# Kernel tuning notes

Measured on AMD Instinct MI355X. Metric: run time of the kernel, lower is better.

The kernel has to match this reference:

```python
import jax, jax.numpy as jnp
import numpy as np

C = 768  # in_channel == out_channel (required by conv9)

def _conv1x1(x, w, b):
    # x: [B,C,H,W], w: [O,C], b: [O]
    return jnp.einsum('bchw,oc->bohw', x, w) + b[None, :, None, None]

def _rot(x):
    # torch: gather with reversed index along dim 3, then permute(0,1,3,2)
    return jnp.swapaxes(jnp.flip(x, axis=3), 2, 3)

def _forward(hidden_states, Ws, bs):
    x = hidden_states
    B, Cc, W, H = x.shape
    o1 = _rot(x); o2 = _rot(o1); o3 = _rot(o2)
    hs11 = (jax.nn.relu(_conv1x1(x,  Ws[0], bs[0]))
          + jax.nn.relu(_conv1x1(o1, Ws[1], bs[1]))
          + jax.nn.relu(_conv1x1(o2, Ws[2], bs[2]))
          + jax.nn.relu(_conv1x1(o3, Ws[3], bs[3])))
    s = W // 2
    e1 = x[:, :, 0:s, 0:s]; e2 = x[:, :, 0:s, s:W]
    e3 = x[:, :, s:W, 0:s]; e4 = x[:, :, s:W, s:W]
    quads = [e1, e2, e3, e4]
    ts = []
    for _ in range(3):
        quads = [_rot(q) for q in quads]
        top = jnp.concatenate((quads[0], quads[1]), axis=-1)
        bot = jnp.concatenate((quads[2], quads[3]), axis=-1)
        ts.append(jnp.concatenate((top, bot), axis=-2))
    hs111 = (jax.nn.relu(_conv1x1(x,     Ws[4], bs[4]))
           + jax.nn.relu(_conv1x1(ts[0], Ws[5], bs[5]))
           + jax.nn.relu(_conv1x1(ts[1], Ws[6], bs[6]))
           + jax.nn.relu(_conv1x1(ts[2], Ws[7], bs[7])))
    # --- spatial matmul attention (per batch & channel, over HxW) ---
    q, k, v = hs11, hs111, hs11
    att = jnp.einsum('bcik,bckj->bcij', q, k)        # [B,C,W,W]
    attn = jax.nn.softmax(att, axis=-1)               # dropout = identity (eval)
    out = jnp.einsum('bcij,bcjh->bcih', attn, v)      # [B,C,W,H]
    out = jax.nn.relu(_conv1x1(out, Ws[8], bs[8]))    # proj dropout = identity (eval)
    return out

def setup_inputs() -> dict:
    key = jax.random.key(0)
    k1, k2, k3 = jax.random.split(key, 3)
    hidden_states = jax.random.normal(k1, (32, C, 32, 32), dtype=jnp.float32)
    # 9 Conv2d(C, C, kernel_size=1) layers -> stacked [9, O, C] weights and [9, O] biases
    fan_in = C
    bound = 1.0 / np.sqrt(fan_in)
    Ws = jax.random.uniform(k2, (9, C, C), minval=-bound, maxval=bound, dtype=jnp.float32)
    bs = jax.random.uniform(k3, (9, C), minval=-bound, maxval=bound, dtype=jnp.float32)
    return {"hidden_states": hidden_states, "Ws": Ws, "bs": bs}

def reference(hidden_states, Ws, bs):
    return _forward(hidden_states, Ws, bs)
```

## Files before the change

kernel.cpp:

```cpp
#include <hip/hip_runtime.h>
#include <hip/hip_fp16.h>

typedef unsigned short u16;
typedef float f32x4 __attribute__((ext_vector_type(4)));
typedef _Float16 half8 __attribute__((ext_vector_type(8)));
typedef unsigned short u16x4 __attribute__((ext_vector_type(4)));

#define CDIM 768
#define NP 1024
#define NB 32

static constexpr size_t CHW = (size_t)NB * CDIM * NP;

static constexpr size_t XT_OFF  = 0;
static constexpr size_t HS_OFF  = CHW * 2;
static constexpr size_t WHI_OFF = HS_OFF + CHW * 4;

__device__ __forceinline__ u16 f16bits(float f) {
  return __half_as_ushort(__float2half_rn(f));
}
__device__ __forceinline__ float f16tof(u16 b) {
  __half_raw hr; hr.x = b; return __half2float(__half(hr));
}

typedef __attribute__((address_space(1))) void gv_t;
typedef __attribute__((address_space(3))) void lv_t;
__device__ __forceinline__ void gload_lds16(const void* g, void* l) {
  __builtin_amdgcn_global_load_lds((gv_t*)g, (lv_t*)l, 16, 0, 0);
}

__global__ __launch_bounds__(256) void cast_w_k(const float* __restrict__ W,
                                                u16* __restrict__ hi) {
  int i = blockIdx.x * 256 + threadIdx.x;
  float4 v = ((const float4*)W)[i];
  u16x4 h4 = {f16bits(v.x), f16bits(v.y), f16bits(v.z), f16bits(v.w)};
  ((u16x4*)hi)[i] = h4;
}

__global__ __launch_bounds__(256) void transpose_f16_k(const float* __restrict__ src,
                                                       u16* __restrict__ dxt) {
  __shared__ float tle[32][33];
  const int b = blockIdx.z, c0 = blockIdx.y * 32, p0 = blockIdx.x * 32;
  const int tid = threadIdx.x;
  const int lr = tid >> 5, lc = tid & 31;
  const float* s = src + ((size_t)b * CDIM + c0) * NP + p0;
#pragma unroll
  for (int it = 0; it < 4; ++it) {
    int c = it * 8 + lr;
    tle[c][lc] = s[(size_t)c * NP + lc];
  }
  __syncthreads();
#pragma unroll
  for (int it = 0; it < 4; ++it) {
    int p = it * 8 + lr;
    float v = tle[lc][p];
    size_t off = ((size_t)b * NP + p0 + p) * CDIM + c0 + lc;
    dxt[off] = f16bits(v);
  }
}

__device__ __forceinline__ int sigma_fn(int mode, int z, int t, int p) {
  if (t == 0 || mode == 1) return p;
  int i = p >> 5, j = p & 31;
  if (z == 0) {
    if (t == 1) return (j << 5) | (31 - i);
    if (t == 2) return ((31 - i) << 5) | (31 - j);
    return ((31 - j) << 5) | i;
  } else {
    int ib = i & 16, jb = j & 16, il = i & 15, jl = j & 15;
    if (t == 1) return ((ib | jl) << 5) | (jb | (15 - il));
    if (t == 2) return ((ib | (15 - il)) << 5) | (jb | (15 - jl));
    return ((ib | (15 - jl)) << 5) | (jb | il);
  }
}

template <int OUTF16>
__global__ __launch_bounds__(512, 2) void gemm_p(
    const u16* __restrict__ Whi,
    const u16* __restrict__ Bx,
    const float* __restrict__ bias, void* __restrict__ dst,
    int nterms, int wselBase, int mode) {
  extern __shared__ u16 lds[];
  const int tid = threadIdx.x;
  const int lane = tid & 63;
  const int w = tid >> 6;
  const int wr = w >> 2, wc = w & 3;
  const int z = blockIdx.z;
  const int b = blockIdx.x >> 2;
  const int p0 = (blockIdx.x & 3) << 8;
  const int o0 = blockIdx.y << 7;
  const int l15 = lane & 15, l4 = lane >> 4;
  const int s7 = l15 & 7;
  float* blds = (float*)(lds + 73728);

  const int NSTEP = nterms * 12;

  const int baseA0 = (wr * 64 + l15) * 64 + ((l4) ^ s7) * 8;
  const int baseA1 = (wr * 64 + l15) * 64 + ((4 + l4) ^ s7) * 8;
  const int baseB0 = 8192 + (wc * 64 + l15) * 32 + (l4 ^ ((l15 >> 1) & 3)) * 8;
  const int baseB1 = baseB0 + 8192;

  int arow[2], acof[2];
#pragma unroll
  for (int it = 0; it < 2; ++it) {
    int d = it * 512 + tid;
    arow[it] = d >> 3;
    acof[it] = ((d & 7) ^ (arow[it] & 7)) * 8;
  }
  int brow[4], bcof[4];
#pragma unroll
  for (int it = 0; it < 4; ++it) {
    int d = it * 512 + tid;
    int h = d >> 10, rem = d & 1023;
    brow[it] = rem >> 2;
    bcof[it] = h * 32 + (((rem & 3) ^ ((brow[it] >> 1) & 3))) * 8;
  }

  const u16* aptr[2];
  const u16* bptr[4];
  auto setPtrs = [&](int term) {
    int wsel = wselBase + z * 4 + term;
#pragma unroll
    for (int it = 0; it < 2; ++it)
      aptr[it] = Whi + ((size_t)wsel * CDIM + o0 + arow[it]) * CDIM + acof[it];
#pragma unroll
    for (int it = 0; it < 4; ++it) {
      int srow = sigma_fn(mode, z, term, p0 + brow[it]);
      bptr[it] = Bx + ((size_t)b * NP + srow) * CDIM + bcof[it];
    }
  };

  if (tid < nterms * 128) {
    int t = tid >> 7, oo = tid & 127;
    blds[tid] = bias[(size_t)(wselBase + z * 4 + t) * CDIM + o0 + oo];
  }
  asm volatile("s_waitcnt lgkmcnt(0)" ::: "memory");

  f32x4 acc[4][4], racc[4][4];
#pragma unroll
  for (int m = 0; m < 4; ++m)
#pragma unroll
    for (int n = 0; n < 4; ++n) {
      acc[m][n] = (f32x4){0.f, 0.f, 0.f, 0.f};
      racc[m][n] = (f32x4){0.f, 0.f, 0.f, 0.f};
    }

  setPtrs(0);
#pragma unroll
  for (int it = 0; it < 2; ++it) gload_lds16(aptr[it], lds + (it * 512 + tid) * 8);
#pragma unroll
  for (int it = 0; it < 4; ++it) gload_lds16(bptr[it], lds + 8192 + (it * 512 + tid) * 8);
#pragma unroll
  for (int it = 0; it < 2; ++it) aptr[it] += 64;
#pragma unroll
  for (int it = 0; it < 4; ++it) bptr[it] += 64;
#pragma unroll
  for (int it = 0; it < 2; ++it) gload_lds16(aptr[it], lds + 24576 + (it * 512 + tid) * 8);
#pragma unroll
  for (int it = 0; it < 4; ++it) gload_lds16(bptr[it], lds + 24576 + 8192 + (it * 512 + tid) * 8);
#pragma unroll
  for (int it = 0; it < 2; ++it) aptr[it] += 64;
#pragma unroll
  for (int it = 0; it < 4; ++it) bptr[it] += 64;

  int nsk = 2, nst = 0;
  int ckk = 0, cterm = 0;
  int cur = 0, wb = 2;

  for (int s = 0; s < NSTEP; ++s) {
    if (s + 1 < NSTEP) {
      asm volatile("s_waitcnt vmcnt(6)" ::: "memory");
    } else {
      asm volatile("s_waitcnt vmcnt(0)" ::: "memory");
    }
    __builtin_amdgcn_s_barrier();
    asm volatile("" ::: "memory");

    const u16* la = lds + cur * 24576;
    u16* ldst = lds + wb * 24576;
    const bool dostage = (s + 2) < NSTEP;
    if (dostage && nsk == 12) { ++nst; nsk = 0; setPtrs(nst); }

    half8 ah[4], bb[4];
#pragma unroll
    for (int m = 0; m < 4; ++m) ah[m] = *(const half8*)(la + baseA0 + m * 1024);
#pragma unroll
    for (int n = 0; n < 4; ++n) bb[n] = *(const half8*)(la + baseB0 + n * 512);
    if (dostage) {
#pragma unroll
      for (int it = 0; it < 2; ++it) gload_lds16(aptr[it], ldst + (it * 512 + tid) * 8);
    }
    asm volatile("s_waitcnt lgkmcnt(0)" ::: "memory");
    __builtin_amdgcn_s_setprio(1);
#pragma unroll
    for (int m = 0; m < 4; ++m)
#pragma unroll
      for (int n = 0; n < 4; ++n)
        acc[m][n] = __builtin_amdgcn_mfma_f32_16x16x32_f16(ah[m], bb[n], acc[m][n], 0, 0, 0);
    __builtin_amdgcn_s_setprio(0);

#pragma unroll
    for (int m = 0; m < 4; ++m) ah[m] = *(const half8*)(la + baseA1 + m * 1024);
#pragma unroll
    for (int n = 0; n < 4; ++n) bb[n] = *(const half8*)(la + baseB1 + n * 512);
    if (dostage) {
#pragma unroll
      for (int it = 0; it < 4; ++it) gload_lds16(bptr[it], ldst + 8192 + (it * 512 + tid) * 8);
#pragma unroll
      for (int it = 0; it < 2; ++it) aptr[it] += 64;
#pragma unroll
      for (int it = 0; it < 4; ++it) bptr[it] += 64;
      ++nsk;
    }
    asm volatile("s_waitcnt lgkmcnt(0)" ::: "memory");
    __builtin_amdgcn_s_setprio(1);
#pragma unroll
    for (int m = 0; m < 4; ++m)
#pragma unroll
      for (int n = 0; n < 4; ++n)
        acc[m][n] = __builtin_amdgcn_mfma_f32_16x16x32_f16(ah[m], bb[n], acc[m][n], 0, 0, 0);
    __builtin_amdgcn_s_setprio(0);

    if (ckk == 11) {
#pragma unroll
      for (int m = 0; m < 4; ++m) {
        float4 bv = *(const float4*)&blds[cterm * 128 + wr * 64 + m * 16 + l4 * 4];
        float bvf[4] = {bv.x, bv.y, bv.z, bv.w};
#pragma unroll
        for (int n = 0; n < 4; ++n)
#pragma unroll
          for (int r = 0; r < 4; ++r) {
            racc[m][n][r] += fmaxf(0.f, acc[m][n][r] + bvf[r]);
            acc[m][n][r] = 0.f;
          }
      }
    }
    cur = cur == 2 ? 0 : cur + 1;
    wb = wb == 2 ? 0 : wb + 1;
    ++ckk; if (ckk == 12) { ckk = 0; ++cterm; }
  }

#pragma unroll
  for (int m = 0; m < 4; ++m) {
    int rowb = o0 + wr * 64 + m * 16 + l4 * 4;
#pragma unroll
    for (int n = 0; n < 4; ++n) {
      int col = p0 + wc * 64 + n * 16 + l15;
      size_t base = ((size_t)b * CDIM + rowb) * NP + col;
      if (OUTF16) {
        u16* dp = (u16*)dst + (size_t)z * CHW + base;
#pragma unroll
        for (int r = 0; r < 4; ++r) dp[(size_t)r * NP] = f16bits(racc[m][n][r]);
      } else {
        float* dp = (float*)dst + (size_t)z * CHW + base;
#pragma unroll
        for (int r = 0; r < 4; ++r) dp[(size_t)r * NP] = racc[m][n][r];
      }
    }
  }
}

__global__ __launch_bounds__(256) void attn_m_k(const u16* __restrict__ hs, u16* __restrict__ aoT) {
  __shared__ float q[4][1024];
  __shared__ float kk[4][1024];
  const int tid = threadIdx.x, w = tid >> 6, lane = tid & 63;
  const int pair0 = blockIdx.x * 4;
  const int b = pair0 / CDIM;
  const int c0 = pair0 % CDIM;
  const int l15 = lane & 15, l4 = lane >> 4;

#pragma unroll
  for (int it = 0; it < 8; ++it) {
    int d4 = it * 256 + tid;
    int pr = d4 >> 9;
    int mat = (d4 >> 8) & 1;
    int off4 = d4 & 255;
    ushort4 hv = *(const ushort4*)&hs[(size_t)mat * CHW + (size_t)(pair0 + pr) * NP + off4 * 4];
    float* dl = mat ? kk[pr] : q[pr];
    int off = off4 * 4;
    int row = off >> 5;
    int ph = ((off & 31) >> 2) ^ (row & 7) ^ (row >> 3);
    float4 v = {f16tof(hv.x), f16tof(hv.y), f16tof(hv.z), f16tof(hv.w)};
    *(float4*)&dl[row * 32 + ph * 4] = v;
  }
  __syncthreads();

  const float* Q = q[w];
  float* KK = kk[w];

  auto rd_row8 = [&](const float* M, int row) -> half8 {
    int rx = (row & 7) ^ (row >> 3);
    float4 a = *(const float4*)&M[row * 32 + ((2 * l4) ^ rx) * 4];
    float4 c = *(const float4*)&M[row * 32 + ((2 * l4 + 1) ^ rx) * 4];
    half8 h;
    h[0] = (_Float16)a.x; h[1] = (_Float16)a.y; h[2] = (_Float16)a.z; h[3] = (_Float16)a.w;
    h[4] = (_Float16)c.x; h[5] = (_Float16)c.y; h[6] = (_Float16)c.z; h[7] = (_Float16)c.w;
    return h;
  };
  auto rd_col8 = [&](const float* M, int col) -> half8 {
    half8 h;
#pragma unroll
    for (int e = 0; e < 8; ++e) {
      int row = l4 * 8 + e;
      int ph = (col >> 2) ^ (row & 7) ^ (row >> 3);
      h[e] = (_Float16)M[row * 32 + ph * 4 + (col & 3)];
    }
    return h;
  };

  half8 bq[2], akk[2];
#pragma unroll
  for (int it = 0; it < 2; ++it) bq[it] = rd_row8(Q, it * 16 + l15);
#pragma unroll
  for (int mh = 0; mh < 2; ++mh) akk[mh] = rd_col8(KK, mh * 16 + l15);
  f32x4 sacc[2][2];
#pragma unroll
  for (int mh = 0; mh < 2; ++mh)
#pragma unroll
    for (int it = 0; it < 2; ++it)
      sacc[mh][it] = __builtin_amdgcn_mfma_f32_16x16x32_f16(
          akk[mh], bq[it], (f32x4){0.f, 0.f, 0.f, 0.f}, 0, 0, 0);

#pragma unroll
  for (int it = 0; it < 2; ++it) {
    float mx = sacc[0][it][0];
#pragma unroll
    for (int r = 1; r < 4; ++r) mx = fmaxf(mx, sacc[0][it][r]);
#pragma unroll
    for (int r = 0; r < 4; ++r) mx = fmaxf(mx, sacc[1][it][r]);
    mx = fmaxf(mx, __shfl_xor(mx, 16));
    mx = fmaxf(mx, __shfl_xor(mx, 32));
    float pv[2][4];
    float sum = 0.f;
#pragma unroll
    for (int mh = 0; mh < 2; ++mh)
#pragma unroll
      for (int r = 0; r < 4; ++r) {
        pv[mh][r] = expf(sacc[mh][it][r] - mx);
        sum += pv[mh][r];
      }
    sum += __shfl_xor(sum, 16);
    sum += __shfl_xor(sum, 32);
    float inv = 1.f / sum;
    int row = it * 16 + l15;
    int rx = (row & 7) ^ (row >> 3);
#pragma unroll
    for (int mh = 0; mh < 2; ++mh) {
      float4 v = {pv[mh][0] * inv, pv[mh][1] * inv, pv[mh][2] * inv, pv[mh][3] * inv};
      *(float4*)&KK[row * 32 + ((mh * 4 + l4) ^ rx) * 4] = v;
    }
  }

  half8 bp[2], av[2];
#pragma unroll
  for (int it = 0; it < 2; ++it) bp[it] = rd_row8(KK, it * 16 + l15);
#pragma unroll
  for (int ht = 0; ht < 2; ++ht) av[ht] = rd_col8(Q, ht * 16 + l15);
  f32x4 oacc[2][2];
#pragma unroll
  for (int ht = 0; ht < 2; ++ht)
#pragma unroll
    for (int it = 0; it < 2; ++it)
      oacc[ht][it] = __builtin_amdgcn_mfma_f32_16x16x32_f16(
          av[ht], bp[it], (f32x4){0.f, 0.f, 0.f, 0.f}, 0, 0, 0);

#pragma unroll
  for (int it = 0; it < 2; ++it) {
    int row = it * 16 + l15;
    int rx = (row & 7) ^ (row >> 3);
#pragma unroll
    for (int ht = 0; ht < 2; ++ht) {
      float4 v = {oacc[ht][it][0], oacc[ht][it][1], oacc[ht][it][2], oacc[ht][it][3]};
      *(float4*)&KK[row * 32 + ((ht * 4 + l4) ^ rx) * 4] = v;
    }
  }
  __syncthreads();

#pragma unroll
  for (int it = 0; it < 4; ++it) {
    int p = it * 256 + tid;
    int row = p >> 5, col = p & 31;
    int idx = row * 32 + (((col >> 2) ^ (row & 7) ^ (row >> 3)) * 4) + (col & 3);
    ushort4 v;
    v.x = f16bits(kk[0][idx]);
    v.y = f16bits(kk[1][idx]);
    v.z = f16bits(kk[2][idx]);
    v.w = f16bits(kk[3][idx]);
    *(ushort4*)&aoT[((size_t)b * NP + p) * CDIM + c0] = v;
  }
}

extern "C" void kernel_launch(void* const* d_in, const int* in_sizes, int n_in,
                              void* d_out, int out_size, void* d_ws, size_t ws_size,
                              hipStream_t stream) {
  (void)in_sizes; (void)n_in; (void)out_size; (void)ws_size;
  const float* x = (const float*)d_in[0];
  const float* Ws = (const float*)d_in[1];
  const float* bs = (const float*)d_in[2];
  float* out = (float*)d_out;
  char* ws = (char*)d_ws;

  u16* XT  = (u16*)(ws + XT_OFF);
  u16* hs  = (u16*)(ws + HS_OFF);
  u16* Whi = (u16*)(ws + WHI_OFF);
  u16* aoT = (u16*)(ws + XT_OFF);

  cast_w_k<<<5184, 256, 0, stream>>>(Ws, Whi);
  transpose_f16_k<<<dim3(32, 24, 32), 256, 0, stream>>>(x, XT);
  gemm_p<1><<<dim3(128, 6, 2), 512, 149504, stream>>>(Whi, XT, bs, (void*)hs, 4, 0, 0);
  attn_m_k<<<6144, 256, 0, stream>>>(hs, aoT);
  gemm_p<0><<<dim3(128, 6, 1), 512, 149504, stream>>>(Whi, aoT, bs, (void*)out, 1, 8, 1);
}
```

Measured before the change: 508.5 us.

## Retile 1x1-conv GEMM to 256x256 blocks with K=32 stages and packed fp16 running sums

```diff
diff --git a/kernel.cpp b/kernel.cpp
--- a/kernel.cpp
+++ b/kernel.cpp
@@ -2,6 +2,7 @@
 #include <hip/hip_fp16.h>
 
 typedef unsigned short u16;
+typedef unsigned int u32;
 typedef float f32x4 __attribute__((ext_vector_type(4)));
 typedef _Float16 half8 __attribute__((ext_vector_type(8)));
 typedef unsigned short u16x4 __attribute__((ext_vector_type(4)));
@@ -21,6 +22,11 @@
 }
 __device__ __forceinline__ float f16tof(u16 b) {
   __half_raw hr; hr.x = b; return __half2float(__half(hr));
+}
+__device__ __forceinline__ u32 pk2(u32 p, float a, float b) {
+  float x = f16tof((u16)(p & 0xffff)) + a;
+  float y = f16tof((u16)(p >> 16)) + b;
+  return (u32)f16bits(x) | ((u32)f16bits(y) << 16);
 }
 
 typedef __attribute__((address_space(1))) void gv_t;
@@ -74,12 +80,12 @@
   }
 }
 
-template <int OUTF16>
-__global__ __launch_bounds__(512, 2) void gemm_p(
+template <int OUTF16, int NTERMS>
+__global__ __launch_bounds__(512, 2) void gemm_r(
     const u16* __restrict__ Whi,
     const u16* __restrict__ Bx,
     const float* __restrict__ bias, void* __restrict__ dst,
-    int nterms, int wselBase, int mode) {
+    int wselBase, int mode) {
   extern __shared__ u16 lds[];
   const int tid = threadIdx.x;
   const int lane = tid & 63;
@@ -88,80 +94,65 @@
   const int z = blockIdx.z;
   const int b = blockIdx.x >> 2;
   const int p0 = (blockIdx.x & 3) << 8;
-  const int o0 = blockIdx.y << 7;
+  const int o0 = blockIdx.y << 8;
   const int l15 = lane & 15, l4 = lane >> 4;
-  const int s7 = l15 & 7;
-  float* blds = (float*)(lds + 73728);
-
-  const int NSTEP = nterms * 12;
-
-  const int baseA0 = (wr * 64 + l15) * 64 + ((l4) ^ s7) * 8;
-  const int baseA1 = (wr * 64 + l15) * 64 + ((4 + l4) ^ s7) * 8;
-  const int baseB0 = 8192 + (wc * 64 + l15) * 32 + (l4 ^ ((l15 >> 1) & 3)) * 8;
-  const int baseB1 = baseB0 + 8192;
-
-  int arow[2], acof[2];
+  float* blds = (float*)(lds + 49152);
+  const int NSTEP = NTERMS * 24;
+
+  const int rA = wr * 128 + l15;
+  const int baseA = rA * 32 + (l4 ^ ((rA >> 1) & 3)) * 8;
+  const int rB = wc * 64 + l15;
+  const int baseB = 8192 + rB * 32 + (l4 ^ ((rB >> 1) & 3)) * 8;
+
+  int srow[2], scof[2];
 #pragma unroll
   for (int it = 0; it < 2; ++it) {
     int d = it * 512 + tid;
-    arow[it] = d >> 3;
-    acof[it] = ((d & 7) ^ (arow[it] & 7)) * 8;
-  }
-  int brow[4], bcof[4];
-#pragma unroll
-  for (int it = 0; it < 4; ++it) {
-    int d = it * 512 + tid;
-    int h = d >> 10, rem = d & 1023;
-    brow[it] = rem >> 2;
-    bcof[it] = h * 32 + (((rem & 3) ^ ((brow[it] >> 1) & 3))) * 8;
-  }
-
+    srow[it] = d >> 2;
+    scof[it] = ((d & 3) ^ ((srow[it] >> 1) & 3)) * 8;
+  }
   const u16* aptr[2];
-  const u16* bptr[4];
+  const u16* bptr[2];
   auto setPtrs = [&](int term) {
     int wsel = wselBase + z * 4 + term;
 #pragma unroll
-    for (int it = 0; it < 2; ++it)
-      aptr[it] = Whi + ((size_t)wsel * CDIM + o0 + arow[it]) * CDIM + acof[it];
-#pragma unroll
-    for (int it = 0; it < 4; ++it) {
-      int srow = sigma_fn(mode, z, term, p0 + brow[it]);
-      bptr[it] = Bx + ((size_t)b * NP + srow) * CDIM + bcof[it];
-    }
-  };
-
-  if (tid < nterms * 128) {
-    int t = tid >> 7, oo = tid & 127;
-    blds[tid] = bias[(size_t)(wselBase + z * 4 + t) * CDIM + o0 + oo];
-  }
+    for (int it = 0; it < 2; ++it) {
+      aptr[it] = Whi + ((size_t)wsel * CDIM + o0 + srow[it]) * CDIM + scof[it];
+      int srw = sigma_fn(mode, z, term, p0 + srow[it]);
+      bptr[it] = Bx + ((size_t)b * NP + srw) * CDIM + scof[it];
+    }
+  };
+  auto stageA = [&](u16* ldst) {
+    gload_lds16(aptr[0], ldst + tid * 8);
+    gload_lds16(aptr[1], ldst + 4096 + tid * 8);
+    aptr[0] += 32; aptr[1] += 32;
+  };
+  auto stageB = [&](u16* ldst) {
+    gload_lds16(bptr[0], ldst + 8192 + tid * 8);
+    gload_lds16(bptr[1], ldst + 12288 + tid * 8);
+    bptr[0] += 32; bptr[1] += 32;
+  };
+
+  for (int i = tid; i < NTERMS * 256; i += 512)
+    blds[i] = bias[(size_t)(wselBase + z * 4 + (i >> 8)) * CDIM + o0 + (i & 255)];
   asm volatile("s_waitcnt lgkmcnt(0)" ::: "memory");
 
-  f32x4 acc[4][4], racc[4][4];
-#pragma unroll
-  for (int m = 0; m < 4; ++m)
-#pragma unroll
-    for (int n = 0; n < 4; ++n) {
-      acc[m][n] = (f32x4){0.f, 0.f, 0.f, 0.f};
-      racc[m][n] = (f32x4){0.f, 0.f, 0.f, 0.f};
-    }
+  f32x4 acc[8][4];
+#pragma unroll
+  for (int mi = 0; mi < 8; ++mi)
+#pragma unroll
+    for (int ni = 0; ni < 4; ++ni) acc[mi][ni] = (f32x4){0.f, 0.f, 0.f, 0.f};
+  u32 rp[8][4][2];
+  if (NTERMS > 1) {
+#pragma unroll
+    for (int mi = 0; mi < 8; ++mi)
+#pragma unroll
+      for (int ni = 0; ni < 4; ++ni) { rp[mi][ni][0] = 0u; rp[mi][ni][1] = 0u; }
+  }
 
   setPtrs(0);
-#pragma unroll
-  for (int it = 0; it < 2; ++it) gload_lds16(aptr[it], lds + (it * 512 + tid) * 8);
-#pragma unroll
-  for (int it = 0; it < 4; ++it) gload_lds16(bptr[it], lds + 8192 + (it * 512 + tid) * 8);
-#pragma unroll
-  for (int it = 0; it < 2; ++it) aptr[it] += 64;
-#pragma unroll
-  for (int it = 0; it < 4; ++it) bptr[it] += 64;
-#pragma unroll
-  for (int it = 0; it < 2; ++it) gload_lds16(aptr[it], lds + 24576 + (it * 512 + tid) * 8);
-#pragma unroll
-  for (int it = 0; it < 4; ++it) gload_lds16(bptr[it], lds + 24576 + 8192 + (it * 512 + tid) * 8);
-#pragma unroll
-  for (int it = 0; it < 2; ++it) aptr[it] += 64;
-#pragma unroll
-  for (int it = 0; it < 4; ++it) bptr[it] += 64;
+  stageA(lds); stageB(lds);
+  stageA(lds + 16384); stageB(lds + 16384);
 
   int nsk = 2, nst = 0;
   int ckk = 0, cterm = 0;
@@ -169,92 +160,84 @@
 
   for (int s = 0; s < NSTEP; ++s) {
     if (s + 1 < NSTEP) {
-      asm volatile("s_waitcnt vmcnt(6)" ::: "memory");
+      asm volatile("s_waitcnt vmcnt(4)" ::: "memory");
     } else {
       asm volatile("s_waitcnt vmcnt(0)" ::: "memory");
     }
     __builtin_amdgcn_s_barrier();
     asm volatile("" ::: "memory");
 
-    const u16* la = lds + cur * 24576;
-    u16* ldst = lds + wb * 24576;
+    const u16* la = lds + cur * 16384;
+    u16* ldst = lds + wb * 16384;
     const bool dostage = (s + 2) < NSTEP;
-    if (dostage && nsk == 12) { ++nst; nsk = 0; setPtrs(nst); }
-
-    half8 ah[4], bb[4];
-#pragma unroll
-    for (int m = 0; m < 4; ++m) ah[m] = *(const half8*)(la + baseA0 + m * 1024);
-#pragma unroll
-    for (int n = 0; n < 4; ++n) bb[n] = *(const half8*)(la + baseB0 + n * 512);
-    if (dostage) {
-#pragma unroll
-      for (int it = 0; it < 2; ++it) gload_lds16(aptr[it], ldst + (it * 512 + tid) * 8);
-    }
+    if (dostage && nsk == 24) { ++nst; nsk = 0; setPtrs(nst); }
+
+    half8 af[4], bf[4];
+#pragma unroll
+    for (int n = 0; n < 4; ++n) bf[n] = *(const half8*)(la + baseB + n * 512);
+#pragma unroll
+    for (int m = 0; m < 4; ++m) af[m] = *(const half8*)(la + baseA + m * 512);
+    if (dostage) stageA(ldst);
     asm volatile("s_waitcnt lgkmcnt(0)" ::: "memory");
     __builtin_amdgcn_s_setprio(1);
 #pragma unroll
     for (int m = 0; m < 4; ++m)
 #pragma unroll
       for (int n = 0; n < 4; ++n)
-        acc[m][n] = __builtin_amdgcn_mfma_f32_16x16x32_f16(ah[m], bb[n], acc[m][n], 0, 0, 0);
+        acc[m][n] = __builtin_amdgcn_mfma_f32_16x16x32_f16(af[m], bf[n], acc[m][n], 0, 0, 0);
     __builtin_amdgcn_s_setprio(0);
 
 #pragma unroll
-    for (int m = 0; m < 4; ++m) ah[m] = *(const half8*)(la + baseA1 + m * 1024);
-#pragma unroll
-    for (int n = 0; n < 4; ++n) bb[n] = *(const half8*)(la + baseB1 + n * 512);
-    if (dostage) {
-#pragma unroll
-      for (int it = 0; it < 4; ++it) gload_lds16(bptr[it], ldst + 8192 + (it * 512 + tid) * 8);
-#pragma unroll
-      for (int it = 0; it < 2; ++it) aptr[it] += 64;
-#pragma unroll
-      for (int it = 0; it < 4; ++it) bptr[it] += 64;
-      ++nsk;
-    }
+    for (int m = 0; m < 4; ++m) af[m] = *(const half8*)(la + baseA + (4 + m) * 512);
+    if (dostage) { stageB(ldst); ++nsk; }
     asm volatile("s_waitcnt lgkmcnt(0)" ::: "memory");
     __builtin_amdgcn_s_setprio(1);
 #pragma unroll
     for (int m = 0; m < 4; ++m)
 #pragma unroll
       for (int n = 0; n < 4; ++n)
-        acc[m][n] = __builtin_amdgcn_mfma_f32_16x16x32_f16(ah[m], bb[n], acc[m][n], 0, 0, 0);
+        acc[4 + m][n] = __builtin_amdgcn_mfma_f32_16x16x32_f16(af[m], bf[n], acc[4 + m][n], 0, 0, 0);
     __builtin_amdgcn_s_setprio(0);
 
-    if (ckk == 11) {
-#pragma unroll
-      for (int m = 0; m < 4; ++m) {
-        float4 bv = *(const float4*)&blds[cterm * 128 + wr * 64 + m * 16 + l4 * 4];
-        float bvf[4] = {bv.x, bv.y, bv.z, bv.w};
-#pragma unroll
-        for (int n = 0; n < 4; ++n)
-#pragma unroll
-          for (int r = 0; r < 4; ++r) {
-            racc[m][n][r] += fmaxf(0.f, acc[m][n][r] + bvf[r]);
-            acc[m][n][r] = 0.f;
-          }
+    if (NTERMS > 1 && ckk == 23) {
+#pragma unroll
+      for (int mi = 0; mi < 8; ++mi) {
+        float4 bv = *(const float4*)&blds[cterm * 256 + wr * 128 + mi * 16 + l4 * 4];
+#pragma unroll
+        for (int ni = 0; ni < 4; ++ni) {
+          rp[mi][ni][0] = pk2(rp[mi][ni][0], fmaxf(0.f, acc[mi][ni][0] + bv.x),
+                                             fmaxf(0.f, acc[mi][ni][1] + bv.y));
+          rp[mi][ni][1] = pk2(rp[mi][ni][1], fmaxf(0.f, acc[mi][ni][2] + bv.z),
+                                             fmaxf(0.f, acc[mi][ni][3] + bv.w));
+          acc[mi][ni] = (f32x4){0.f, 0.f, 0.f, 0.f};
+        }
       }
     }
     cur = cur == 2 ? 0 : cur + 1;
     wb = wb == 2 ? 0 : wb + 1;
-    ++ckk; if (ckk == 12) { ckk = 0; ++cterm; }
-  }
-
-#pragma unroll
-  for (int m = 0; m < 4; ++m) {
-    int rowb = o0 + wr * 64 + m * 16 + l4 * 4;
-#pragma unroll
-    for (int n = 0; n < 4; ++n) {
-      int col = p0 + wc * 64 + n * 16 + l15;
+    ++ckk; if (ckk == 24) { ckk = 0; ++cterm; }
+  }
+
+#pragma unroll
+  for (int mi = 0; mi < 8; ++mi) {
+    int rowb = o0 + wr * 128 + mi * 16 + l4 * 4;
+#pragma unroll
+    for (int ni = 0; ni < 4; ++ni) {
+      int col = p0 + wc * 64 + ni * 16 + l15;
       size_t base = ((size_t)b * CDIM + rowb) * NP + col;
-      if (OUTF16) {
+      if (NTERMS > 1) {
         u16* dp = (u16*)dst + (size_t)z * CHW + base;
-#pragma unroll
-        for (int r = 0; r < 4; ++r) dp[(size_t)r * NP] = f16bits(racc[m][n][r]);
+        dp[0 * NP] = (u16)(rp[mi][ni][0] & 0xffff);
+        dp[1 * NP] = (u16)(rp[mi][ni][0] >> 16);
+        dp[2 * NP] = (u16)(rp[mi][ni][1] & 0xffff);
+        dp[3 * NP] = (u16)(rp[mi][ni][1] >> 16);
       } else {
+        float4 bv = *(const float4*)&blds[wr * 128 + mi * 16 + l4 * 4];
+        float bvf[4] = {bv.x, bv.y, bv.z, bv.w};
         float* dp = (float*)dst + (size_t)z * CHW + base;
 #pragma unroll
-        for (int r = 0; r < 4; ++r) dp[(size_t)r * NP] = racc[m][n][r];
+        for (int r = 0; r < 4; ++r)
+          dp[(size_t)r * NP] = fmaxf(0.f, acc[mi][ni][r] + bvf[r]);
       }
     }
   }
@@ -407,7 +390,7 @@
 
   cast_w_k<<<5184, 256, 0, stream>>>(Ws, Whi);
   transpose_f16_k<<<dim3(32, 24, 32), 256, 0, stream>>>(x, XT);
-  gemm_p<1><<<dim3(128, 6, 2), 512, 149504, stream>>>(Whi, XT, bs, (void*)hs, 4, 0, 0);
+  gemm_r<1, 4><<<dim3(128, 3, 2), 512, 102400, stream>>>(Whi, XT, bs, (void*)hs, 0, 0);
   attn_m_k<<<6144, 256, 0, stream>>>(hs, aoT);
-  gemm_p<0><<<dim3(128, 6, 1), 512, 149504, stream>>>(Whi, aoT, bs, (void*)out, 1, 8, 1);
-}
+  gemm_r<0, 1><<<dim3(128, 3, 1), 512, 99328, stream>>>(Whi, aoT, bs, (void*)out, 8, 1);
+}
```

Measured after the change: 503.9 us. No clear change (-0.9%).

## Block activations into 16-channel panels, rewrite attention and add dedicated final GEMM

Applied to the files above, without the earlier changes.

```diff
diff --git a/kernel.cpp b/kernel.cpp
--- a/kernel.cpp
+++ b/kernel.cpp
@@ -2,6 +2,7 @@
 #include <hip/hip_fp16.h>
 
 typedef unsigned short u16;
+typedef unsigned int u32;
 typedef float f32x4 __attribute__((ext_vector_type(4)));
 typedef _Float16 half8 __attribute__((ext_vector_type(8)));
 typedef unsigned short u16x4 __attribute__((ext_vector_type(4)));
@@ -10,7 +11,8 @@
 #define NP 1024
 #define NB 32
 
-static constexpr size_t CHW = (size_t)NB * CDIM * NP;
+static constexpr size_t PBATCH = (size_t)CDIM * NP;
+static constexpr size_t CHW = (size_t)NB * PBATCH;
 
 static constexpr size_t XT_OFF  = 0;
 static constexpr size_t HS_OFF  = CHW * 2;
@@ -22,6 +24,7 @@
 __device__ __forceinline__ float f16tof(u16 b) {
   __half_raw hr; hr.x = b; return __half2float(__half(hr));
 }
+__device__ __forceinline__ int akey(int r) { return ((r >> 1) & 3) ^ ((r >> 3) & 3); }
 
 typedef __attribute__((address_space(1))) void gv_t;
 typedef __attribute__((address_space(3))) void lv_t;
@@ -52,9 +55,10 @@
   __syncthreads();
 #pragma unroll
   for (int it = 0; it < 4; ++it) {
-    int p = it * 8 + lr;
-    float v = tle[lc][p];
-    size_t off = ((size_t)b * NP + p0 + p) * CDIM + c0 + lc;
+    int p = p0 + it * 8 + lr;
+    float v = tle[lc][it * 8 + lr];
+    int c = c0 + lc;
+    size_t off = (size_t)b * PBATCH + (size_t)(c >> 4) * (NP * 16) + (size_t)p * 16 + (c & 15);
     dxt[off] = f16bits(v);
   }
 }
@@ -126,7 +130,8 @@
 #pragma unroll
     for (int it = 0; it < 4; ++it) {
       int srow = sigma_fn(mode, z, term, p0 + brow[it]);
-      bptr[it] = Bx + ((size_t)b * NP + srow) * CDIM + bcof[it];
+      int cc = bcof[it];
+      bptr[it] = Bx + (size_t)b * PBATCH + (size_t)(cc >> 4) * (NP * 16) + (size_t)srow * 16 + (cc & 15);
     }
   };
 
@@ -153,7 +158,7 @@
 #pragma unroll
   for (int it = 0; it < 2; ++it) aptr[it] += 64;
 #pragma unroll
-  for (int it = 0; it < 4; ++it) bptr[it] += 64;
+  for (int it = 0; it < 4; ++it) bptr[it] += 65536;
 #pragma unroll
   for (int it = 0; it < 2; ++it) gload_lds16(aptr[it], lds + 24576 + (it * 512 + tid) * 8);
 #pragma unroll
@@ -161,7 +166,7 @@
 #pragma unroll
   for (int it = 0; it < 2; ++it) aptr[it] += 64;
 #pragma unroll
-  for (int it = 0; it < 4; ++it) bptr[it] += 64;
+  for (int it = 0; it < 4; ++it) bptr[it] += 65536;
 
   int nsk = 2, nst = 0;
   int ckk = 0, cterm = 0;
@@ -209,7 +214,7 @@
 #pragma unroll
       for (int it = 0; it < 2; ++it) aptr[it] += 64;
 #pragma unroll
-      for (int it = 0; it < 4; ++it) bptr[it] += 64;
+      for (int it = 0; it < 4; ++it) bptr[it] += 65536;
       ++nsk;
     }
     asm volatile("s_waitcnt lgkmcnt(0)" ::: "memory");
@@ -260,59 +265,172 @@
   }
 }
 
-__global__ __launch_bounds__(256) void attn_m_k(const u16* __restrict__ hs, u16* __restrict__ aoT) {
-  __shared__ float q[4][1024];
-  __shared__ float kk[4][1024];
+__global__ __launch_bounds__(512, 2) void gemm_r(
+    const u16* __restrict__ Whi,
+    const u16* __restrict__ Bx,
+    const float* __restrict__ bias, float* __restrict__ dst,
+    int wselBase) {
+  extern __shared__ u16 lds[];
+  const int tid = threadIdx.x;
+  const int lane = tid & 63;
+  const int w = tid >> 6;
+  const int wr = w >> 2, wc = w & 3;
+  const int b = blockIdx.x >> 2;
+  const int p0 = (blockIdx.x & 3) << 8;
+  const int o0 = blockIdx.y << 8;
+  const int l15 = lane & 15, l4 = lane >> 4;
+  float* blds = (float*)(lds + 49152);
+  const int NSTEP = 24;
+
+  const int rA = wr * 128 + l15;
+  const int baseA = rA * 32 + (l4 ^ ((rA >> 1) & 3)) * 8;
+  const int rB = wc * 64 + l15;
+  const int baseB = 8192 + rB * 32 + (l4 ^ ((rB >> 1) & 3)) * 8;
+
+  int srow[2], scof[2];
+#pragma unroll
+  for (int it = 0; it < 2; ++it) {
+    int d = it * 512 + tid;
+    srow[it] = d >> 2;
+    scof[it] = ((d & 3) ^ ((srow[it] >> 1) & 3)) * 8;
+  }
+  const u16* aptr[2];
+  const u16* bptr[2];
+  {
+    int wsel = wselBase;
+#pragma unroll
+    for (int it = 0; it < 2; ++it) {
+      aptr[it] = Whi + ((size_t)wsel * CDIM + o0 + srow[it]) * CDIM + scof[it];
+      int cc = scof[it];
+      bptr[it] = Bx + (size_t)b * PBATCH + (size_t)(cc >> 4) * (NP * 16) + (size_t)(p0 + srow[it]) * 16 + (cc & 15);
+    }
+  }
+  auto stageA = [&](u16* ldst) {
+    gload_lds16(aptr[0], ldst + tid * 8);
+    gload_lds16(aptr[1], ldst + 4096 + tid * 8);
+    aptr[0] += 32; aptr[1] += 32;
+  };
+  auto stageB = [&](u16* ldst) {
+    gload_lds16(bptr[0], ldst + 8192 + tid * 8);
+    gload_lds16(bptr[1], ldst + 12288 + tid * 8);
+    bptr[0] += 32768; bptr[1] += 32768;
+  };
+
+  for (int i = tid; i < 256; i += 512)
+    blds[i] = bias[(size_t)wselBase * CDIM + o0 + i];
+  asm volatile("s_waitcnt lgkmcnt(0)" ::: "memory");
+
+  f32x4 acc[8][4];
+#pragma unroll
+  for (int mi = 0; mi < 8; ++mi)
+#pragma unroll
+    for (int ni = 0; ni < 4; ++ni) acc[mi][ni] = (f32x4){0.f, 0.f, 0.f, 0.f};
+
+  stageA(lds); stageB(lds);
+  stageA(lds + 16384); stageB(lds + 16384);
+
+  int cur = 0, wb = 2;
+  for (int s = 0; s < NSTEP; ++s) {
+    if (s + 1 < NSTEP) {
+      asm volatile("s_waitcnt vmcnt(4)" ::: "memory");
+    } else {
+      asm volatile("s_waitcnt vmcnt(0)" ::: "memory");
+    }
+    __builtin_amdgcn_s_barrier();
+    asm volatile("" ::: "memory");
+
+    const u16* la = lds + cur * 16384;
+    u16* ldst = lds + wb * 16384;
+    const bool dostage = (s + 2) < NSTEP;
+
+    half8 af[4], bf[4];
+#pragma unroll
+    for (int n = 0; n < 4; ++n) bf[n] = *(const half8*)(la + baseB + n * 512);
+#pragma unroll
+    for (int m = 0; m < 4; ++m) af[m] = *(const half8*)(la + baseA + m * 512);
+    if (dostage) stageA(ldst);
+    asm volatile("s_waitcnt lgkmcnt(0)" ::: "memory");
+    __builtin_amdgcn_s_setprio(1);
+#pragma unroll
+    for (int m = 0; m < 4; ++m)
+#pragma unroll
+      for (int n = 0; n < 4; ++n)
+        acc[m][n] = __builtin_amdgcn_mfma_f32_16x16x32_f16(af[m], bf[n], acc[m][n], 0, 0, 0);
+    __builtin_amdgcn_s_setprio(0);
+
+#pragma unroll
+    for (int m = 0; m < 4; ++m) af[m] = *(const half8*)(la + baseA + (4 + m) * 512);
+    if (dostage) stageB(ldst);
+    asm volatile("s_waitcnt lgkmcnt(0)" ::: "memory");
+    __builtin_amdgcn_s_setprio(1);
+#pragma unroll
+    for (int m = 0; m < 4; ++m)
+#pragma unroll
+      for (int n = 0; n < 4; ++n)
+        acc[4 + m][n] = __builtin_amdgcn_mfma_f32_16x16x32_f16(af[m], bf[n], acc[4 + m][n], 0, 0, 0);
+    __builtin_amdgcn_s_setprio(0);
+
+    cur = cur == 2 ? 0 : cur + 1;
+    wb = wb == 2 ? 0 : wb + 1;
+  }
+
+#pragma unroll
+  for (int mi = 0; mi < 8; ++mi) {
+    int rowb = o0 + wr * 128 + mi * 16 + l4 * 4;
+    float4 bv = *(const float4*)&blds[wr * 128 + mi * 16 + l4 * 4];
+    float bvf[4] = {bv.x, bv.y, bv.z, bv.w};
+#pragma unroll
+    for (int ni = 0; ni < 4; ++ni) {
+      int col = p0 + wc * 64 + ni * 16 + l15;
+      float* dp = dst + ((size_t)b * CDIM + rowb) * NP + col;
+#pragma unroll
+      for (int r = 0; r < 4; ++r)
+        dp[(size_t)r * NP] = fmaxf(0.f, acc[mi][ni][r] + bvf[r]);
+    }
+  }
+}
+
+__global__ __launch_bounds__(1024) void attn_t_k(const u16* __restrict__ hs, u16* __restrict__ aoT) {
+  extern __shared__ u16 att[];
   const int tid = threadIdx.x, w = tid >> 6, lane = tid & 63;
-  const int pair0 = blockIdx.x * 4;
+  const int pair0 = blockIdx.x * 16;
   const int b = pair0 / CDIM;
   const int c0 = pair0 % CDIM;
   const int l15 = lane & 15, l4 = lane >> 4;
 
 #pragma unroll
-  for (int it = 0; it < 8; ++it) {
-    int d4 = it * 256 + tid;
-    int pr = d4 >> 9;
-    int mat = (d4 >> 8) & 1;
-    int off4 = d4 & 255;
-    ushort4 hv = *(const ushort4*)&hs[(size_t)mat * CHW + (size_t)(pair0 + pr) * NP + off4 * 4];
-    float* dl = mat ? kk[pr] : q[pr];
-    int off = off4 * 4;
-    int row = off >> 5;
-    int ph = ((off & 31) >> 2) ^ (row & 7) ^ (row >> 3);
-    float4 v = {f16tof(hv.x), f16tof(hv.y), f16tof(hv.z), f16tof(hv.w)};
-    *(float4*)&dl[row * 32 + ph * 4] = v;
-  }
+  for (int it = 0; it < 4; ++it) {
+    int d = it * 1024 + tid;
+    int pair = d >> 8, mat = (d >> 7) & 1, rem = d & 127;
+    int r = rem >> 2, ph = rem & 3;
+    int ch = ph ^ akey(r);
+    const u16* src = hs + (size_t)mat * CHW + (size_t)(pair0 + pair) * NP + r * 32 + ch * 8;
+    gload_lds16(src, att + (size_t)d * 8);
+  }
+  asm volatile("s_waitcnt vmcnt(0)" ::: "memory");
   __syncthreads();
 
-  const float* Q = q[w];
-  float* KK = kk[w];
-
-  auto rd_row8 = [&](const float* M, int row) -> half8 {
-    int rx = (row & 7) ^ (row >> 3);
-    float4 a = *(const float4*)&M[row * 32 + ((2 * l4) ^ rx) * 4];
-    float4 c = *(const float4*)&M[row * 32 + ((2 * l4 + 1) ^ rx) * 4];
-    half8 h;
-    h[0] = (_Float16)a.x; h[1] = (_Float16)a.y; h[2] = (_Float16)a.z; h[3] = (_Float16)a.w;
-    h[4] = (_Float16)c.x; h[5] = (_Float16)c.y; h[6] = (_Float16)c.z; h[7] = (_Float16)c.w;
-    return h;
+  u16* Qb = att + w * 2048;
+  u16* Kb = Qb + 1024;
+
+  auto rd_row8 = [&](const u16* M, int row) -> half8 {
+    return *(const half8*)(M + row * 32 + (l4 ^ akey(row)) * 8);
   };
-  auto rd_col8 = [&](const float* M, int col) -> half8 {
-    half8 h;
+  auto rd_col8 = [&](const u16* M, int col) -> half8 {
+    union { u16 u[8]; half8 h; } t;
 #pragma unroll
     for (int e = 0; e < 8; ++e) {
       int row = l4 * 8 + e;
-      int ph = (col >> 2) ^ (row & 7) ^ (row >> 3);
-      h[e] = (_Float16)M[row * 32 + ph * 4 + (col & 3)];
-    }
-    return h;
+      t.u[e] = M[row * 32 + ((col >> 3) ^ akey(row)) * 8 + (col & 7)];
+    }
+    return t.h;
   };
 
   half8 bq[2], akk[2];
 #pragma unroll
-  for (int it = 0; it < 2; ++it) bq[it] = rd_row8(Q, it * 16 + l15);
-#pragma unroll
-  for (int mh = 0; mh < 2; ++mh) akk[mh] = rd_col8(KK, mh * 16 + l15);
+  for (int it = 0; it < 2; ++it) bq[it] = rd_row8(Qb, it * 16 + l15);
+#pragma unroll
+  for (int mh = 0; mh < 2; ++mh) akk[mh] = rd_col8(Kb, mh * 16 + l15);
   f32x4 sacc[2][2];
 #pragma unroll
   for (int mh = 0; mh < 2; ++mh)
@@ -343,19 +461,22 @@
     sum += __shfl_xor(sum, 32);
     float inv = 1.f / sum;
     int row = it * 16 + l15;
-    int rx = (row & 7) ^ (row >> 3);
+    int rk = akey(row);
 #pragma unroll
     for (int mh = 0; mh < 2; ++mh) {
-      float4 v = {pv[mh][0] * inv, pv[mh][1] * inv, pv[mh][2] * inv, pv[mh][3] * inv};
-      *(float4*)&KK[row * 32 + ((mh * 4 + l4) ^ rx) * 4] = v;
+      int c = mh * 16 + l4 * 4;
+      uint2 wv;
+      wv.x = (u32)f16bits(pv[mh][0] * inv) | ((u32)f16bits(pv[mh][1] * inv) << 16);
+      wv.y = (u32)f16bits(pv[mh][2] * inv) | ((u32)f16bits(pv[mh][3] * inv) << 16);
+      *(uint2*)(Kb + row * 32 + ((c >> 3) ^ rk) * 8 + (c & 7)) = wv;
     }
   }
 
   half8 bp[2], av[2];
 #pragma unroll
-  for (int it = 0; it < 2; ++it) bp[it] = rd_row8(KK, it * 16 + l15);
-#pragma unroll
-  for (int ht = 0; ht < 2; ++ht) av[ht] = rd_col8(Q, ht * 16 + l15);
+  for (int it = 0; it < 2; ++it) bp[it] = rd_row8(Kb, it * 16 + l15);
+#pragma unroll
+  for (int ht = 0; ht < 2; ++ht) av[ht] = rd_col8(Qb, ht * 16 + l15);
   f32x4 oacc[2][2];
 #pragma unroll
   for (int ht = 0; ht < 2; ++ht)
@@ -367,26 +488,30 @@
 #pragma unroll
   for (int it = 0; it < 2; ++it) {
     int row = it * 16 + l15;
-    int rx = (row & 7) ^ (row >> 3);
+    int rk = akey(row);
 #pragma unroll
     for (int ht = 0; ht < 2; ++ht) {
-      float4 v = {oacc[ht][it][0], oacc[ht][it][1], oacc[ht][it][2], oacc[ht][it][3]};
-      *(float4*)&KK[row * 32 + ((ht * 4 + l4) ^ rx) * 4] = v;
+      int c = ht * 16 + l4 * 4;
+      uint2 wv;
+      wv.x = (u32)f16bits(oacc[ht][it][0]) | ((u32)f16bits(oacc[ht][it][1]) << 16);
+      wv.y = (u32)f16bits(oacc[ht][it][2]) | ((u32)f16bits(oacc[ht][it][3]) << 16);
+      *(uint2*)(Qb + row * 32 + ((c >> 3) ^ rk) * 8 + (c & 7)) = wv;
     }
   }
   __syncthreads();
 
 #pragma unroll
   for (int it = 0; it < 4; ++it) {
-    int p = it * 256 + tid;
-    int row = p >> 5, col = p & 31;
-    int idx = row * 32 + (((col >> 2) ^ (row & 7) ^ (row >> 3)) * 4) + (col & 3);
+    int s = it * 1024 + tid;
+    int p = s >> 2, cq = s & 3;
+    int row = p >> 5, colh = p & 31;
+    int boff = row * 32 + ((colh >> 3) ^ akey(row)) * 8 + (colh & 7);
     ushort4 v;
-    v.x = f16bits(kk[0][idx]);
-    v.y = f16bits(kk[1][idx]);
-    v.z = f16bits(kk[2][idx]);
-    v.w = f16bits(kk[3][idx]);
-    *(ushort4*)&aoT[((size_t)b * NP + p) * CDIM + c0] = v;
+    v.x = att[(cq * 4 + 0) * 2048 + boff];
+    v.y = att[(cq * 4 + 1) * 2048 + boff];
+    v.z = att[(cq * 4 + 2) * 2048 + boff];
+    v.w = att[(cq * 4 + 3) * 2048 + boff];
+    *(ushort4*)&aoT[(size_t)b * PBATCH + (size_t)(c0 >> 4) * (NP * 16) + (size_t)p * 16 + cq * 4] = v;
   }
 }
 
@@ -408,6 +533,6 @@
   cast_w_k<<<5184, 256, 0, stream>>>(Ws, Whi);
   transpose_f16_k<<<dim3(32, 24, 32), 256, 0, stream>>>(x, XT);
   gemm_p<1><<<dim3(128, 6, 2), 512, 149504, stream>>>(Whi, XT, bs, (void*)hs, 4, 0, 0);
-  attn_m_k<<<6144, 256, 0, stream>>>(hs, aoT);
-  gemm_p<0><<<dim3(128, 6, 1), 512, 149504, stream>>>(Whi, aoT, bs, (void*)out, 1, 8, 1);
-}
+  attn_t_k<<<1536, 1024, 65536, stream>>>(hs, aoT);
+  gemm_r<<<dim3(128, 3, 1), 512, 99328, stream>>>(Whi, aoT, bs, out, 8);
+}
```

Measured after the change: 464.8 us. 8.6% less time.
